# Kernel optimization log

Hardware: AMD Instinct MI355X
Metric: run time of the kernel (lower is better)

Reference implementation:

```python
import jax, jax.numpy as jnp
import numpy as np

B, T, D = 32, 400, 64
EPS = 1e-6


def setup_inputs() -> dict:
    key = jax.random.key(0)
    k1, k2, k3 = jax.random.split(key, 3)
    x = jax.random.normal(k1, (B, T, D), dtype=jnp.float32)
    mu = jax.random.normal(k2, (B, T, D), dtype=jnp.float32)
    # Build SPD covariance matrices: A A^T / D + I
    A = jax.random.normal(k3, (B, T, D, D), dtype=jnp.float32)
    sigma = jnp.einsum('btij,btkj->btik', A, A) / D + jnp.eye(D, dtype=jnp.float32)
    return {"x": x, "mu": mu, "sigma": sigma}


def reference(x, mu, sigma):
    d = sigma.shape[-1]
    # Regularize and factorize: sigma + eps*I = L L^T
    L = jnp.linalg.cholesky(sigma + EPS * jnp.eye(d, dtype=sigma.dtype))  # [B,T,D,D]
    diff = x - mu  # [B,T,D]
    # Solve L z = diff (batched lower-triangular solve)
    z = jax.scipy.linalg.solve_triangular(L, diff[..., None], lower=True)[..., 0]  # [B,T,D]
    log_det = jnp.sum(jnp.log(jnp.diagonal(L, axis1=-2, axis2=-1)), axis=-1)  # [B,T]
    log_prob = -0.5 * jnp.sum(z * z, axis=-1) - log_det - 0.5 * d * jnp.log(2.0 * jnp.pi)
    ll = jnp.mean(jnp.sum(log_prob, axis=1), axis=0)  # sum over time, mean over batch
    return jnp.expand_dims(-ll, axis=-1)  # shape [1]
```

## Files before the change

kernel.cpp:

```cpp
#include <hip/hip_runtime.h>

#define D_   64
#define NBT_ 12800
#define B_   32

__device__ __forceinline__ float rl(float v, int l) {
    return __uint_as_float(__builtin_amdgcn_readlane(__float_as_uint(v), l));
}

__global__ __launch_bounds__(256) void chol_ll(const float* __restrict__ x,
                                               const float* __restrict__ mu,
                                               const float* __restrict__ sigma,
                                               float* __restrict__ partial) {
    const int lane = threadIdx.x & 63;
    const int wv   = threadIdx.x >> 6;
    const int bt   = blockIdx.x * 4 + wv;

    const float4* srow = (const float4*)(sigma + (size_t)bt * (D_ * D_) + (size_t)lane * D_);
    float row[D_];
    #pragma unroll
    for (int m = 0; m < D_ / 4; ++m) {
        float4 t = srow[m];
        row[4 * m + 0] = t.x; row[4 * m + 1] = t.y;
        row[4 * m + 2] = t.z; row[4 * m + 3] = t.w;
    }
    float d = x[bt * D_ + lane] - mu[bt * D_ + lane];

    float q = 0.f, lg = 0.f;
    #pragma unroll
    for (int k = 0; k < D_; ++k) {
        float s   = rl(row[k], k) + 1e-6f;
        float inv = __builtin_amdgcn_rsqf(s);
        lg += __builtin_amdgcn_logf(s);
        row[k] *= inv;
        float zk = rl(d, k) * inv;
        q += zk * zk;
        d -= row[k] * zk;
        #pragma unroll
        for (int j = k + 1; j < D_; ++j)
            row[j] -= row[k] * rl(row[k], j);
    }
    if (lane == 0) {
        float log_det = 0.34657359027997264f * lg;
        float lp = -0.5f * q - log_det - 58.81206612509905f;
        partial[bt] = lp;
    }
}

__global__ __launch_bounds__(1024) void reduce_ll(const float* __restrict__ partial,
                                                  float* __restrict__ out) {
    float s = 0.f;
    for (int i = threadIdx.x; i < NBT_; i += 1024) s += partial[i];
    #pragma unroll
    for (int off = 32; off > 0; off >>= 1) s += __shfl_down(s, off, 64);
    __shared__ float ws[16];
    const int lane = threadIdx.x & 63, w = threadIdx.x >> 6;
    if (lane == 0) ws[w] = s;
    __syncthreads();
    if (threadIdx.x == 0) {
        float t = 0.f;
        #pragma unroll
        for (int i = 0; i < 16; ++i) t += ws[i];
        out[0] = -t / (float)B_;
    }
}

extern "C" void kernel_launch(void* const* d_in, const int* in_sizes, int n_in,
                              void* d_out, int out_size, void* d_ws, size_t ws_size,
                              hipStream_t stream) {
    const float* x     = (const float*)d_in[0];
    const float* mu    = (const float*)d_in[1];
    const float* sigma = (const float*)d_in[2];
    float* partial = (float*)d_ws;
    chol_ll<<<NBT_ / 4, 256, 0, stream>>>(x, mu, sigma, partial);
    reduce_ll<<<1, 1024, 0, stream>>>(partial, (float*)d_out);
}
```

Before: 338.9 us.

## Broadcast Cholesky column via LDS and use packed float2 FMA updates

Replaces the per-element readlane broadcast in the trailing Cholesky update with a write of the scaled column to a double-buffered LDS slot, followed by float4 LDS reads. The row state is held as float2 vectors so the rank-1 update can use packed FMA instructions. The aim is to cut the scalar readlane and SALU-to-VALU traffic in the inner loop. In exchange it adds LDS stores and loads each step and relies on in-wave ordering without a barrier. Updating whole 4-wide groups from (k+1)>>2 also touches already-finished columns, which is harmless only because those entries are never read again.

```diff
diff --git a/kernel.cpp b/kernel.cpp
--- a/kernel.cpp
+++ b/kernel.cpp
@@ -4,42 +4,61 @@
 #define NBT_ 12800
 #define B_   32
 
+typedef float v2f __attribute__((ext_vector_type(2)));
+typedef float v4f __attribute__((ext_vector_type(4)));
+
 __device__ __forceinline__ float rl(float v, int l) {
     return __uint_as_float(__builtin_amdgcn_readlane(__float_as_uint(v), l));
 }
 
-__global__ __launch_bounds__(256) void chol_ll(const float* __restrict__ x,
-                                               const float* __restrict__ mu,
-                                               const float* __restrict__ sigma,
-                                               float* __restrict__ partial) {
+__global__ __launch_bounds__(256, 4) void chol_ll(const float* __restrict__ x,
+                                                  const float* __restrict__ mu,
+                                                  const float* __restrict__ sigma,
+                                                  float* __restrict__ partial) {
     const int lane = threadIdx.x & 63;
     const int wv   = threadIdx.x >> 6;
     const int bt   = blockIdx.x * 4 + wv;
 
-    const float4* srow = (const float4*)(sigma + (size_t)bt * (D_ * D_) + (size_t)lane * D_);
-    float row[D_];
+    __shared__ __align__(16) float colbuf[4][2][D_];
+    float* const cb0 = colbuf[wv][0];
+    float* const cb1 = colbuf[wv][1];
+
+    const v4f* srow = (const v4f*)(sigma + (size_t)bt * (D_ * D_) + (size_t)lane * D_);
+    v2f row[D_ / 2];
     #pragma unroll
     for (int m = 0; m < D_ / 4; ++m) {
-        float4 t = srow[m];
-        row[4 * m + 0] = t.x; row[4 * m + 1] = t.y;
-        row[4 * m + 2] = t.z; row[4 * m + 3] = t.w;
+        v4f t = srow[m];
+        row[2 * m]     = (v2f){t[0], t[1]};
+        row[2 * m + 1] = (v2f){t[2], t[3]};
     }
     float d = x[bt * D_ + lane] - mu[bt * D_ + lane];
 
     float q = 0.f, lg = 0.f;
     #pragma unroll
     for (int k = 0; k < D_; ++k) {
-        float s   = rl(row[k], k) + 1e-6f;
+        float rk  = row[k >> 1][k & 1];
+        float s   = rl(rk, k) + 1e-6f;
         float inv = __builtin_amdgcn_rsqf(s);
         lg += __builtin_amdgcn_logf(s);
-        row[k] *= inv;
+        float a = rk * inv;
         float zk = rl(d, k) * inv;
         q += zk * zk;
-        d -= row[k] * zk;
-        #pragma unroll
-        for (int j = k + 1; j < D_; ++j)
-            row[j] -= row[k] * rl(row[k], j);
+        d -= a * zk;
+
+        if (k < D_ - 1) {
+            float* cb = (k & 1) ? cb1 : cb0;
+            cb[lane] = a;
+            const v2f av = {a, a};
+            const int m0 = (k + 1) >> 2;
+            #pragma unroll
+            for (int m = m0; m < D_ / 4; ++m) {
+                v4f bc = *(const v4f*)(cb + 4 * m);
+                row[2 * m]     -= av * (v2f){bc[0], bc[1]};
+                row[2 * m + 1] -= av * (v2f){bc[2], bc[3]};
+            }
+        }
     }
+
     if (lane == 0) {
         float log_det = 0.34657359027997264f * lg;
         float lp = -0.5f * q - log_det - 58.81206612509905f;
```

Result: slower. 359.0 us (+5.9%).

## Block Cholesky update by 4 columns using LDS broadcast instead of readlanes

Applied to the files above, without the earlier changes.

Restructures the per-wave Cholesky into panels of four columns. Each panel is factored with readlanes, then written to a double-buffered LDS region so the trailing update reads four multipliers per row with one vector LDS load, replacing one scalar readlane per element. It also sets a minimum-occupancy launch bound. The cost is LDS traffic, added shared memory per block, and possible register pressure from the occupancy hint.

```diff
diff --git a/kernel.cpp b/kernel.cpp
--- a/kernel.cpp
+++ b/kernel.cpp
@@ -4,17 +4,23 @@
 #define NBT_ 12800
 #define B_   32
 
+typedef float v4f __attribute__((ext_vector_type(4)));
+
 __device__ __forceinline__ float rl(float v, int l) {
     return __uint_as_float(__builtin_amdgcn_readlane(__float_as_uint(v), l));
 }
 
-__global__ __launch_bounds__(256) void chol_ll(const float* __restrict__ x,
-                                               const float* __restrict__ mu,
-                                               const float* __restrict__ sigma,
-                                               float* __restrict__ partial) {
+__global__ __launch_bounds__(256, 2) void chol_ll(const float* __restrict__ x,
+                                                  const float* __restrict__ mu,
+                                                  const float* __restrict__ sigma,
+                                                  float* __restrict__ partial) {
     const int lane = threadIdx.x & 63;
     const int wv   = threadIdx.x >> 6;
     const int bt   = blockIdx.x * 4 + wv;
+
+    __shared__ __align__(16) float colbuf[4][2][4 * D_];
+    float* const cb0 = colbuf[wv][0];
+    float* const cb1 = colbuf[wv][1];
 
     const float4* srow = (const float4*)(sigma + (size_t)bt * (D_ * D_) + (size_t)lane * D_);
     float row[D_];
@@ -28,18 +34,42 @@
 
     float q = 0.f, lg = 0.f;
     #pragma unroll
-    for (int k = 0; k < D_; ++k) {
-        float s   = rl(row[k], k) + 1e-6f;
-        float inv = __builtin_amdgcn_rsqf(s);
-        lg += __builtin_amdgcn_logf(s);
-        row[k] *= inv;
-        float zk = rl(d, k) * inv;
-        q += zk * zk;
-        d -= row[k] * zk;
+    for (int g = 0; g < D_ / 4; ++g) {
+        const int k0 = 4 * g;
+
         #pragma unroll
-        for (int j = k + 1; j < D_; ++j)
-            row[j] -= row[k] * rl(row[k], j);
+        for (int p = 0; p < 4; ++p) {
+            const int kp = k0 + p;
+            #pragma unroll
+            for (int pp = 0; pp < p; ++pp)
+                row[kp] -= row[k0 + pp] * rl(row[k0 + pp], kp);
+            float s   = rl(row[kp], kp) + 1e-6f;
+            float inv = __builtin_amdgcn_rsqf(s);
+            lg += __builtin_amdgcn_logf(s);
+            row[kp] *= inv;
+            float zk = rl(d, kp) * inv;
+            q += zk * zk;
+            d -= row[kp] * zk;
+        }
+
+        if (g < D_ / 4 - 1) {
+            float* cb = (g & 1) ? cb1 : cb0;
+            *(v4f*)(cb + 4 * lane) =
+                (v4f){row[k0], row[k0 + 1], row[k0 + 2], row[k0 + 3]};
+
+            #pragma unroll
+            for (int m = g + 1; m < D_ / 4; ++m) {
+                #pragma unroll
+                for (int jj = 0; jj < 4; ++jj) {
+                    const int j = 4 * m + jj;
+                    v4f b = *(const v4f*)(cb + 4 * j);
+                    row[j] -= row[k0]     * b[0] + row[k0 + 1] * b[1]
+                            + row[k0 + 2] * b[2] + row[k0 + 3] * b[3];
+                }
+            }
+        }
     }
+
     if (lane == 0) {
         float log_det = 0.34657359027997264f * lg;
         float lp = -0.5f * q - log_det - 58.81206612509905f;
```

Result: faster. 312.2 us (-7.9%).
